# Kernel tuning notes

Measured on AMD Instinct MI355X. Metric: run time of the kernel, lower is better.

## Reference

```python
import jax, jax.numpy as jnp
import numpy as np
from jax import lax

H = W = 512
NT = 1000


def setup_inputs() -> dict:
    key = jax.random.key(0)
    kx, ky = jax.random.split(key)
    X = jax.random.uniform(kx, (H, W), dtype=jnp.float32)
    Y = jax.random.uniform(ky, (H, W), dtype=jnp.float32)
    return {"X": X, "Y": Y}


def reference(X, Y):
    # Gaussian initial condition, same math as torch.exp(-50*((X-0.5)^2+(Y-0.5)^2))
    x0 = jnp.exp(-50.0 * ((X - 0.5) ** 2 + (Y - 0.5) ** 2))
    h, w = x0.shape
    # mask zeroing the boundary (rows/cols 0 and -1)
    mask = jnp.zeros((h, w), dtype=x0.dtype).at[1:-1, 1:-1].set(1.0)

    def step(x, _):
        # 3x3 cross kernel [[0,.25,0],[.25,0,.25],[0,.25,0]] with zero padding=1,
        # expressed as four shifted adds (identical math, no conv launch overhead)
        p = jnp.pad(x, 1)
        xn = 0.25 * (p[:-2, 1:-1] + p[2:, 1:-1] + p[1:-1, :-2] + p[1:-1, 2:])
        return xn * mask, None

    x, _ = lax.scan(step, x0, None, length=NT)
    # original returns NCHW with N=C=1
    return x[None, None]
```

## Files before the change

### kernel.cpp

```cpp
#include <hip/hip_runtime.h>
#include <math.h>


#define HW 512
#define NP 64
#define NC 32

__device__ __forceinline__ int mode_of(int p) {
    return (p < NC) ? (p + 1) : (p + 447);
}

__device__ __forceinline__ float gauss(const float* __restrict__ X,
                                       const float* __restrict__ Y, int idx) {
    float dx = X[idx] - 0.5f, dy = Y[idx] - 0.5f;
    return expf(-50.0f * (dx * dx + dy * dy));
}

__global__ void k_prep(const float* __restrict__ X, const float* __restrict__ Y,
                       float* __restrict__ x1, float* __restrict__ S,
                       float* __restrict__ ST) {
    int b = blockIdx.x, t = threadIdx.x;
    if (b < 1024) {
        int idx = b * 256 + t;
        int i = idx >> 9, j = idx & 511;
        float v = 0.0f;
        if (i > 0 && i < HW - 1 && j > 0 && j < HW - 1) {
            v = 0.25f * (gauss(X, Y, idx - HW) + gauss(X, Y, idx + HW) +
                         gauss(X, Y, idx - 1)  + gauss(X, Y, idx + 1));
        }
        x1[idx] = v;
    } else {
        int idx = (b - 1024) * 256 + t;
        int pa = idx >> 9, i = idx & 511;
        long tt = ((long)(pa + 1) * (long)i) % 1022;
        float s = (float)sin((double)tt * (M_PI / 511.0));
        float sm = (i & 1) ? s : -s;
        S[pa * HW + i] = s;
        S[(63 - pa) * HW + i] = sm;
        ST[i * NP + pa] = s;
        ST[i * NP + (63 - pa)] = sm;
    }
}

__global__ void k_m1(const float* __restrict__ S, const float* __restrict__ x1,
                     float* __restrict__ P) {
    int j = blockIdx.x * 256 + threadIdx.x;
    int p0 = blockIdx.y * 8;
    int iz = blockIdx.z;
    int i0 = iz * 32;
    const float* Sb = S + p0 * HW + i0;
    const float* xp = x1 + i0 * HW + j;
    float a[8] = {0.f, 0.f, 0.f, 0.f, 0.f, 0.f, 0.f, 0.f};
    #pragma unroll 8
    for (int i = 0; i < 32; i++) {
        float x = xp[i * HW];
        #pragma unroll
        for (int k = 0; k < 8; k++) a[k] += Sb[k * HW + i] * x;
    }
    float* Pp = P + iz * NP * HW + p0 * HW + j;
    #pragma unroll
    for (int k = 0; k < 8; k++) Pp[k * HW] = a[k];
}

__global__ void k_m23(const float* __restrict__ P, const float* __restrict__ ST,
                      const float* __restrict__ S, float* __restrict__ E) {
    __shared__ float c1[HW];
    __shared__ float part[512];
    __shared__ float drow[NP];
    int p = blockIdx.x, t = threadIdx.x;
    {
        const float* Pp = P + p * HW + t;
        float s0 = 0.f, s1 = 0.f;
        #pragma unroll
        for (int iz = 0; iz < 16; iz += 2) {
            s0 += Pp[iz * NP * HW];
            s1 += Pp[(iz + 1) * NP * HW];
        }
        c1[t] = s0 + s1;
    }
    __syncthreads();
    int q = t & 63, jg = t >> 6;
    {
        const float* STp = ST + (jg * 64) * NP + q;
        const float* cc = c1 + jg * 64;
        float b0 = 0.f, b1 = 0.f;
        #pragma unroll 8
        for (int j = 0; j < 64; j += 2) {
            b0 += cc[j] * STp[j * NP];
            b1 += cc[j + 1] * STp[(j + 1) * NP];
        }
        part[t] = b0 + b1;
    }
    __syncthreads();
    if (t < NP) {
        float ps = 0.f;
        #pragma unroll
        for (int g = 0; g < 8; g++) ps += part[t + 64 * g];
        double lp = cos((double)mode_of(p) * M_PI / 511.0);
        double lq = cos((double)mode_of(t) * M_PI / 511.0);
        double lam = 0.5 * (lp + lq);
        double r = 1.0, base = fabs(lam);
        int e = 999;
        #pragma unroll
        for (int k = 0; k < 10; k++) {
            if (e & 1) r *= base;
            base *= base;
            e >>= 1;
        }
        if (lam < 0.0) r = -r;
        drow[t] = ps * (float)(r * (2.0 / 511.0) * (2.0 / 511.0));
    }
    __syncthreads();
    float e0 = 0.f, e1 = 0.f;
    #pragma unroll 8
    for (int qq = 0; qq < NP; qq += 2) {
        e0 += drow[qq] * S[qq * HW + t];
        e1 += drow[qq + 1] * S[(qq + 1) * HW + t];
    }
    E[p * HW + t] = e0 + e1;
}

__global__ void k_m4(const float* __restrict__ S, const float* __restrict__ E,
                     float* __restrict__ out) {
    int j = blockIdx.x * 256 + threadIdx.x;
    int i0 = blockIdx.y * 4;
    float a0 = 0.f, a1 = 0.f, a2 = 0.f, a3 = 0.f;
    #pragma unroll 16
    for (int p = 0; p < NP; p++) {
        float e = E[p * HW + j];
        a0 += S[p * HW + i0 + 0] * e;
        a1 += S[p * HW + i0 + 1] * e;
        a2 += S[p * HW + i0 + 2] * e;
        a3 += S[p * HW + i0 + 3] * e;
    }
    out[(i0 + 0) * HW + j] = a0;
    out[(i0 + 1) * HW + j] = a1;
    out[(i0 + 2) * HW + j] = a2;
    out[(i0 + 3) * HW + j] = a3;
}


extern "C" void kernel_launch(void* const* d_in, const int* in_sizes, int n_in,
                              void* d_out, int out_size, void* d_ws, size_t ws_size,
                              hipStream_t stream) {
    const float* X = (const float*)d_in[0];
    const float* Y = (const float*)d_in[1];
    float* out = (float*)d_out;

    float* ws = (float*)d_ws;
    float* x1 = ws;
    float* S  = x1 + HW * HW;
    float* ST = S + NP * HW;
    float* E  = ST + HW * NP;
    float* P  = E + NP * HW;

    k_prep<<<dim3(1088),        dim3(256), 0, stream>>>(X, Y, x1, S, ST);
    k_m1  <<<dim3(2, 8, 16),    dim3(256), 0, stream>>>(S, x1, P);
    k_m23 <<<dim3(NP),          dim3(512), 0, stream>>>(P, ST, S, E);
    k_m4  <<<dim3(2, 128),      dim3(256), 0, stream>>>(S, E, out);
}
```

Before: 72.43 us.

## Exploit even/odd symmetry of sine modes to halve spectral transform work

The truncated sine-basis transform now stores only the 32 low modes and rebuilds the 32 high modes from the parity relation S[63-pa][i] = ±S[pa][i], splitting the sums into even and odd index halves. This roughly halves the multiply-adds and basis loads in k_m1, k_m23 and k_m4. k_m1 is re-split into 32 i-chunks of 16 with 4 mode groups, so k_m23 now reduces 32 partial slabs. The cost is extra adds/subtracts and more partial-sum traffic in P.

```diff
diff --git a/kernel.cpp b/kernel.cpp
--- a/kernel.cpp
+++ b/kernel.cpp
@@ -34,88 +34,110 @@
         int pa = idx >> 9, i = idx & 511;
         long tt = ((long)(pa + 1) * (long)i) % 1022;
         float s = (float)sin((double)tt * (M_PI / 511.0));
-        float sm = (i & 1) ? s : -s;
         S[pa * HW + i] = s;
-        S[(63 - pa) * HW + i] = sm;
-        ST[i * NP + pa] = s;
-        ST[i * NP + (63 - pa)] = sm;
+        ST[i * NC + pa] = s;
     }
 }
 
 __global__ void k_m1(const float* __restrict__ S, const float* __restrict__ x1,
                      float* __restrict__ P) {
     int j = blockIdx.x * 256 + threadIdx.x;
-    int p0 = blockIdx.y * 8;
+    int pa0 = blockIdx.y * 8;
     int iz = blockIdx.z;
-    int i0 = iz * 32;
-    const float* Sb = S + p0 * HW + i0;
+    int i0 = iz * 16;
+    const float* Sb = S + pa0 * HW + i0;
     const float* xp = x1 + i0 * HW + j;
-    float a[8] = {0.f, 0.f, 0.f, 0.f, 0.f, 0.f, 0.f, 0.f};
-    #pragma unroll 8
-    for (int i = 0; i < 32; i++) {
+    float ae[8] = {0.f, 0.f, 0.f, 0.f, 0.f, 0.f, 0.f, 0.f};
+    float ao[8] = {0.f, 0.f, 0.f, 0.f, 0.f, 0.f, 0.f, 0.f};
+    #pragma unroll
+    for (int i = 0; i < 16; i++) {
         float x = xp[i * HW];
-        #pragma unroll
-        for (int k = 0; k < 8; k++) a[k] += Sb[k * HW + i] * x;
+        if ((i & 1) == 0) {
+            #pragma unroll
+            for (int k = 0; k < 8; k++) ae[k] += Sb[k * HW + i] * x;
+        } else {
+            #pragma unroll
+            for (int k = 0; k < 8; k++) ao[k] += Sb[k * HW + i] * x;
+        }
     }
-    float* Pp = P + iz * NP * HW + p0 * HW + j;
+    float* Pp = P + iz * NP * HW + j;
     #pragma unroll
-    for (int k = 0; k < 8; k++) Pp[k * HW] = a[k];
+    for (int k = 0; k < 8; k++) {
+        Pp[(pa0 + k) * HW]      = ae[k] + ao[k];
+        Pp[(63 - pa0 - k) * HW] = ao[k] - ae[k];
+    }
 }
 
 __global__ void k_m23(const float* __restrict__ P, const float* __restrict__ ST,
                       const float* __restrict__ S, float* __restrict__ E) {
     __shared__ float c1[HW];
-    __shared__ float part[512];
-    __shared__ float drow[NP];
+    __shared__ float pe[512], po[512];
+    __shared__ float dp[NC], dm[NC];
     int p = blockIdx.x, t = threadIdx.x;
     {
         const float* Pp = P + p * HW + t;
-        float s0 = 0.f, s1 = 0.f;
+        float s0 = 0.f, s1 = 0.f, s2 = 0.f, s3 = 0.f;
         #pragma unroll
-        for (int iz = 0; iz < 16; iz += 2) {
-            s0 += Pp[iz * NP * HW];
+        for (int iz = 0; iz < 32; iz += 4) {
+            s0 += Pp[(iz + 0) * NP * HW];
             s1 += Pp[(iz + 1) * NP * HW];
+            s2 += Pp[(iz + 2) * NP * HW];
+            s3 += Pp[(iz + 3) * NP * HW];
         }
-        c1[t] = s0 + s1;
+        c1[t] = (s0 + s1) + (s2 + s3);
     }
     __syncthreads();
-    int q = t & 63, jg = t >> 6;
+    int qa = t & 31, jg = t >> 5;
     {
-        const float* STp = ST + (jg * 64) * NP + q;
-        const float* cc = c1 + jg * 64;
-        float b0 = 0.f, b1 = 0.f;
-        #pragma unroll 8
-        for (int j = 0; j < 64; j += 2) {
-            b0 += cc[j] * STp[j * NP];
-            b1 += cc[j + 1] * STp[(j + 1) * NP];
+        const float* STp = ST + (jg * 32) * NC + qa;
+        const float* cc = c1 + jg * 32;
+        float be = 0.f, bo = 0.f;
+        #pragma unroll
+        for (int jj = 0; jj < 32; jj += 2) {
+            be += cc[jj] * STp[jj * NC];
+            bo += cc[jj + 1] * STp[(jj + 1) * NC];
         }
-        part[t] = b0 + b1;
+        pe[t] = be;
+        po[t] = bo;
     }
     __syncthreads();
-    if (t < NP) {
-        float ps = 0.f;
+    if (t < NC) {
+        float se = 0.f, so = 0.f;
         #pragma unroll
-        for (int g = 0; g < 8; g++) ps += part[t + 64 * g];
+        for (int g = 0; g < 16; g++) {
+            se += pe[g * 32 + t];
+            so += po[g * 32 + t];
+        }
+        float dlo = se + so;
+        float dhi = so - se;
         double lp = cos((double)mode_of(p) * M_PI / 511.0);
-        double lq = cos((double)mode_of(t) * M_PI / 511.0);
-        double lam = 0.5 * (lp + lq);
-        double r = 1.0, base = fabs(lam);
+        double ca = cos((double)(t + 1) * M_PI / 511.0);
+        double lam1 = 0.5 * (lp + ca);
+        double lam2 = 0.5 * (lp - ca);
+        double r1 = 1.0, b1 = fabs(lam1);
+        double r2 = 1.0, b2 = fabs(lam2);
         int e = 999;
         #pragma unroll
         for (int k = 0; k < 10; k++) {
-            if (e & 1) r *= base;
-            base *= base;
+            if (e & 1) { r1 *= b1; r2 *= b2; }
+            b1 *= b1; b2 *= b2;
             e >>= 1;
         }
-        if (lam < 0.0) r = -r;
-        drow[t] = ps * (float)(r * (2.0 / 511.0) * (2.0 / 511.0));
+        if (lam1 < 0.0) r1 = -r1;
+        if (lam2 < 0.0) r2 = -r2;
+        const double sc = (2.0 / 511.0) * (2.0 / 511.0);
+        dlo *= (float)(r1 * sc);
+        dhi *= (float)(r2 * sc);
+        dp[t] = dlo + dhi;
+        dm[t] = dlo - dhi;
     }
     __syncthreads();
+    const float* sel = (t & 1) ? dp : dm;
     float e0 = 0.f, e1 = 0.f;
-    #pragma unroll 8
-    for (int qq = 0; qq < NP; qq += 2) {
-        e0 += drow[qq] * S[qq * HW + t];
-        e1 += drow[qq + 1] * S[(qq + 1) * HW + t];
+    #pragma unroll
+    for (int q2 = 0; q2 < NC; q2 += 2) {
+        e0 += sel[q2] * S[q2 * HW + t];
+        e1 += sel[q2 + 1] * S[(q2 + 1) * HW + t];
     }
     E[p * HW + t] = e0 + e1;
 }
@@ -125,13 +147,16 @@
     int j = blockIdx.x * 256 + threadIdx.x;
     int i0 = blockIdx.y * 4;
     float a0 = 0.f, a1 = 0.f, a2 = 0.f, a3 = 0.f;
-    #pragma unroll 16
-    for (int p = 0; p < NP; p++) {
-        float e = E[p * HW + j];
-        a0 += S[p * HW + i0 + 0] * e;
-        a1 += S[p * HW + i0 + 1] * e;
-        a2 += S[p * HW + i0 + 2] * e;
-        a3 += S[p * HW + i0 + 3] * e;
+    #pragma unroll 8
+    for (int pa = 0; pa < NC; pa++) {
+        float elo = E[pa * HW + j];
+        float ehi = E[(63 - pa) * HW + j];
+        float ep = elo + ehi, em = elo - ehi;
+        const float* Sp = S + pa * HW + i0;
+        a0 += Sp[0] * em;
+        a1 += Sp[1] * ep;
+        a2 += Sp[2] * em;
+        a3 += Sp[3] * ep;
     }
     out[(i0 + 0) * HW + j] = a0;
     out[(i0 + 1) * HW + j] = a1;
@@ -150,12 +175,12 @@
     float* ws = (float*)d_ws;
     float* x1 = ws;
     float* S  = x1 + HW * HW;
-    float* ST = S + NP * HW;
-    float* E  = ST + HW * NP;
+    float* ST = S + NC * HW;
+    float* E  = ST + HW * NC;
     float* P  = E + NP * HW;
 
     k_prep<<<dim3(1088),        dim3(256), 0, stream>>>(X, Y, x1, S, ST);
-    k_m1  <<<dim3(2, 8, 16),    dim3(256), 0, stream>>>(S, x1, P);
+    k_m1  <<<dim3(2, 4, 32),    dim3(256), 0, stream>>>(S, x1, P);
     k_m23 <<<dim3(NP),          dim3(512), 0, stream>>>(P, ST, S, E);
     k_m4  <<<dim3(2, 128),      dim3(256), 0, stream>>>(S, E, out);
 }
```

New measurement: 70.60 us, median of 2. -2.5%, faster.
